# Kernel tuning notes

Measured on AMD Instinct MI355X. Metric: run time of the kernel, lower is better.

Reference implementation:

```python
import jax, jax.numpy as jnp
import numpy as np

B, S = 32, 128
E_NUM, SKILL, D_K, D_E, D_A = 4000, 256, 128, 128, 128
AT_NUM, IT_NUM = 1000, 1000
GAMMA = 0.03


def _lin(key, out_d, in_d):
    # xavier-normal style init
    w = jax.random.normal(key, (out_d, in_d), jnp.float32) * (2.0 / (in_d + out_d)) ** 0.5
    b = jnp.zeros((out_d,), jnp.float32)
    return w, b


def setup_inputs() -> dict:
    key = jax.random.key(0)
    ks = jax.random.split(key, 16)
    exercise_id = jax.random.randint(ks[0], (B, S), 0, E_NUM, jnp.int32)
    ans_time = jax.random.randint(ks[1], (B, S), 0, AT_NUM, jnp.int32)
    interval_time = jax.random.randint(ks[2], (B, S), 0, IT_NUM, jnp.int32)
    answer_value = jax.random.randint(ks[3], (B, S), 0, 2, jnp.int32)
    # enhanced q-matrix: binary with zeros replaced by gamma
    qmask = jax.random.bernoulli(ks[4], 0.1, (E_NUM, SKILL))
    q_matrix = jnp.where(qmask, 1.0, GAMMA).astype(jnp.float32)
    ex_table = jax.random.normal(ks[5], (E_NUM, D_E), jnp.float32)
    at_table = jax.random.normal(ks[6], (AT_NUM, D_K), jnp.float32)
    it_table = jax.random.normal(ks[7], (IT_NUM, D_K), jnp.float32)
    W1, b1 = _lin(ks[8], D_K, D_E + D_K + D_A)   # learning_embed_layer
    Wl, bl = _lin(ks[9], D_K, 4 * D_K)           # learning_layer
    Wg, bg = _lin(ks[10], D_K, 4 * D_K)          # learning_gate
    Wf, bf = _lin(ks[11], D_K, 3 * D_K)          # forgetting_gate
    Wp, bp = _lin(ks[12], D_K, 2 * D_K)          # predicting_layer
    # xavier-uniform initial knowledge state, shared across batch
    lim = (6.0 / (SKILL + D_K)) ** 0.5
    h0 = jax.random.uniform(ks[13], (SKILL, D_K), jnp.float32, -lim, lim)
    return {"exercise_id": exercise_id, "ans_time": ans_time,
            "interval_time": interval_time, "answer_value": answer_value,
            "q_matrix": q_matrix, "ex_table": ex_table, "at_table": at_table,
            "it_table": it_table, "W1": W1, "b1": b1, "Wl": Wl, "bl": bl,
            "Wg": Wg, "bg": bg, "Wf": Wf, "bf": bf, "Wp": Wp, "bp": bp, "h0": h0}


def _forward(exercise_id, ans_time, interval_time, answer_value, q_matrix,
             ex_table, at_table, it_table, W1, b1, Wl, bl, Wg, bg, Wf, bf,
             Wp, bp, h0):
    b, s = exercise_id.shape
    ex = ex_table[exercise_id]                       # (B,S,d_e)
    at = at_table[ans_time]                          # (B,S,d_k)
    it = it_table[interval_time]                     # (B,S,d_k)
    ans = jnp.broadcast_to(answer_value.astype(ex.dtype)[..., None], (b, s, D_A))
    le = jnp.concatenate([ex, at, ans], -1) @ W1.T + b1   # learning embedding (B,S,d_k)
    kv = q_matrix[exercise_id]                       # knowledge vectors (B,S,skill)

    h_pre = jnp.broadcast_to(h0, (b,) + h0.shape)    # (B,skill,d_k)
    h_tilde_pre = jnp.einsum('bs,bsd->bd', kv[:, 0], h_pre)
    learning_pre = jnp.zeros((b, D_K), ex.dtype)

    def step(carry, xs):
        h_pre, h_tilde_pre, learning_pre = carry
        lv, itv, kv_t, kv_next, ex_next = xs
        x4 = jnp.concatenate([learning_pre, itv, lv, h_tilde_pre], -1)
        lg = jnp.tanh(x4 @ Wl.T + bl)
        gate = jax.nn.sigmoid(x4 @ Wg.T + bg)
        LG = gate * (lg + 1.0) * 0.5                 # (B,d_k)
        LG_tilde = kv_t[:, :, None] * LG[:, None, :] # outer product addressing (B,skill,d_k)
        x3 = jnp.concatenate([h_pre,
                              jnp.broadcast_to(LG[:, None, :], h_pre.shape),
                              jnp.broadcast_to(itv[:, None, :], h_pre.shape)], -1)
        f = jax.nn.sigmoid(x3 @ Wf.T + bf)           # forget gate per skill
        h = LG_tilde + f * h_pre                     # updated knowledge state
        h_tilde = jnp.einsum('bs,bsd->bd', kv_next, h)
        pred = jax.nn.sigmoid(jnp.concatenate([ex_next, h_tilde], -1) @ Wp.T + bp)
        return (h, h_tilde, lv), pred

    sw = lambda a: jnp.swapaxes(a, 0, 1)
    xs = (sw(le[:, :-1]), sw(it[:, 1:]), sw(kv[:, :-1]), sw(kv[:, 1:]), sw(ex[:, 1:]))
    _, preds = jax.lax.scan(step, (h_pre, h_tilde_pre, learning_pre), xs)
    return jnp.swapaxes(preds, 0, 1)                 # (B, S-1, d_k)


def reference(exercise_id, ans_time, interval_time, answer_value, q_matrix,
              ex_table, at_table, it_table, W1, b1, Wl, bl, Wg, bg, Wf, bf,
              Wp, bp, h0):
    return _forward(exercise_id, ans_time, interval_time, answer_value, q_matrix,
                    ex_table, at_table, it_table, W1, b1, Wl, bl, Wg, bg, Wf, bf,
                    Wp, bp, h0)
```

## Files before the change

### kernel.cpp

```cpp
#include <hip/hip_runtime.h>

typedef unsigned int u32;
typedef unsigned short u16;
typedef u16 u16x8 __attribute__((ext_vector_type(8)));
typedef u16 u16x4 __attribute__((ext_vector_type(4)));
typedef __bf16 bf16x8 __attribute__((ext_vector_type(8)));
typedef __bf16 bf16x4v __attribute__((ext_vector_type(4)));
typedef float f32x4 __attribute__((ext_vector_type(4)));
typedef float f32x2 __attribute__((ext_vector_type(2)));

#define B_SZ 32
#define S_SZ 128
#define T_SZ 127
#define DK 128
#define SKILL 256
#define SQTR 64
#define RL 136
#define PP 68
#define NPAIR 8

__device__ __forceinline__ u16x4 cvt4(f32x4 v) {
    return __builtin_bit_cast(u16x4, __builtin_convertvector(v, bf16x4v));
}
__device__ __forceinline__ u16x8 cvt8(f32x4 a, f32x4 b) {
    u16x4 x = cvt4(a), y = cvt4(b);
    u16x8 r;
    r[0]=x[0]; r[1]=x[1]; r[2]=x[2]; r[3]=x[3];
    r[4]=y[0]; r[5]=y[1]; r[6]=y[2]; r[7]=y[3];
    return r;
}
__device__ __forceinline__ u16 bfu(float x) {
    return __builtin_bit_cast(u16, (__bf16)x);
}
__device__ __forceinline__ float sigm(float x) {
    float e = __builtin_amdgcn_exp2f(-1.44269504f * x);
    return __builtin_amdgcn_rcpf(1.f + e);
}
__device__ __forceinline__ float tanh_f(float x) {
    float e = __builtin_amdgcn_exp2f(-2.88539008f * x);
    return 2.f * __builtin_amdgcn_rcpf(1.f + e) - 1.f;
}
__device__ __forceinline__ f32x4 mfma16(u16x8 a, u16x8 bb, f32x4 c) {
    return __builtin_amdgcn_mfma_f32_16x16x32_bf16(
        __builtin_bit_cast(bf16x8, a), __builtin_bit_cast(bf16x8, bb), c, 0, 0, 0);
}

__global__ __launch_bounds__(256) void k_le(
    const int* __restrict__ eid, const int* __restrict__ atime,
    const int* __restrict__ ansv, const float* __restrict__ ex_t,
    const float* __restrict__ at_t, const float* __restrict__ W1,
    const float* __restrict__ b1, float* __restrict__ le_ws)
{
    __shared__ float xS[NPAIR * 256];
    __shared__ int   eS[NPAIR], aS[NPAIR];
    __shared__ float avS[NPAIR];
    const int tid = threadIdx.x;
    const int p0 = blockIdx.x * NPAIR;
    if (tid < NPAIR) {
        int p = p0 + tid;
        int b = p / T_SZ, t = p - b * T_SZ;
        eS[tid] = eid[b * S_SZ + t];
        aS[tid] = atime[b * S_SZ + t];
        avS[tid] = (float)ansv[b * S_SZ + t];
    }
    __syncthreads();
    #pragma unroll
    for (int it = 0; it < 2; ++it) {
        int f = it * 256 + tid;
        int pr = f >> 6, c = f & 63;
        const float* src = (c < 32) ? ex_t + eS[pr] * DK + 4 * c
                                    : at_t + aS[pr] * DK + 4 * (c - 32);
        *(f32x4*)(xS + pr * 256 + 4 * c) = *(const f32x4*)src;
    }
    __syncthreads();
    const int o = tid & 127, g = tid >> 7;
    const float* wr = W1 + o * 384;
    const float bias = b1[o];
    float acc[4];
    #pragma unroll
    for (int i = 0; i < 4; ++i) acc[i] = bias;
    #pragma unroll 2
    for (int k4 = 0; k4 < 64; ++k4) {
        f32x4 w = *(const f32x4*)(wr + 4 * k4);
        #pragma unroll
        for (int i = 0; i < 4; ++i) {
            f32x4 x = *(const f32x4*)(xS + (g * 4 + i) * 256 + 4 * k4);
            acc[i] += w[0] * x[0] + w[1] * x[1] + w[2] * x[2] + w[3] * x[3];
        }
    }
    float wsum = 0.f;
    #pragma unroll 4
    for (int k4 = 64; k4 < 96; ++k4) {
        f32x4 w = *(const f32x4*)(wr + 4 * k4);
        wsum += w[0] + w[1] + w[2] + w[3];
    }
    #pragma unroll
    for (int i = 0; i < 4; ++i) {
        int p = p0 + g * 4 + i;
        le_ws[p * DK + o] = acc[i] + avS[g * 4 + i] * wsum;
    }
}

__global__ __launch_bounds__(256) void k_pre(
    const int* __restrict__ itime, const float* __restrict__ it_t,
    const float* __restrict__ Wl, const float* __restrict__ blv,
    const float* __restrict__ Wg, const float* __restrict__ bgv,
    const float* __restrict__ Wf, const float* __restrict__ bfv,
    const float* __restrict__ le_ws,
    float* __restrict__ PRE_l, float* __restrict__ PRE_g, float* __restrict__ PRE_f)
{
    __shared__ float xS[NPAIR * 384];
    __shared__ int ivS[NPAIR], t0S[NPAIR];
    const int tid = threadIdx.x;
    const int p0 = blockIdx.x * NPAIR;
    if (tid < NPAIR) {
        int p = p0 + tid;
        int b = p / T_SZ, t = p - b * T_SZ;
        ivS[tid] = itime[b * S_SZ + t + 1];
        t0S[tid] = (t == 0);
    }
    __syncthreads();
    #pragma unroll
    for (int it = 0; it < 3; ++it) {
        int f = it * 256 + tid;
        int pr = f / 96, c = f - pr * 96;
        int p = p0 + pr;
        f32x4 v;
        if (c < 32) {
            v = t0S[pr] ? (f32x4){0.f, 0.f, 0.f, 0.f}
                        : *(const f32x4*)(le_ws + (p - 1) * DK + 4 * c);
        } else if (c < 64) {
            v = *(const f32x4*)(it_t + ivS[pr] * DK + 4 * (c - 32));
        } else {
            v = *(const f32x4*)(le_ws + p * DK + 4 * (c - 64));
        }
        *(f32x4*)(xS + pr * 384 + 4 * c) = v;
    }
    __syncthreads();
    const int o = tid & 127, g = tid >> 7;
    const float* wl = Wl + o * 512;
    const float* wg = Wg + o * 512;
    const float bl0 = blv[o], bg0 = bgv[o];
    float al[4], ag[4];
    #pragma unroll
    for (int i = 0; i < 4; ++i) { al[i] = bl0; ag[i] = bg0; }
    #pragma unroll 2
    for (int k4 = 0; k4 < 96; ++k4) {
        f32x4 w  = *(const f32x4*)(wl + 4 * k4);
        f32x4 w2 = *(const f32x4*)(wg + 4 * k4);
        #pragma unroll
        for (int i = 0; i < 4; ++i) {
            f32x4 x = *(const f32x4*)(xS + (g * 4 + i) * 384 + 4 * k4);
            al[i] += w[0] * x[0] + w[1] * x[1] + w[2] * x[2] + w[3] * x[3];
            ag[i] += w2[0] * x[0] + w2[1] * x[1] + w2[2] * x[2] + w2[3] * x[3];
        }
    }
    const float bf0 = bfv[o];
    float af[4];
    #pragma unroll
    for (int i = 0; i < 4; ++i) af[i] = bf0;
    const float* wf = Wf + o * 384 + 256;
    #pragma unroll 2
    for (int k4 = 0; k4 < 32; ++k4) {
        f32x4 w = *(const f32x4*)(wf + 4 * k4);
        #pragma unroll
        for (int i = 0; i < 4; ++i) {
            f32x4 x = *(const f32x4*)(xS + (g * 4 + i) * 384 + 128 + 4 * k4);
            af[i] += w[0] * x[0] + w[1] * x[1] + w[2] * x[2] + w[3] * x[3];
        }
    }
    #pragma unroll
    for (int i = 0; i < 4; ++i) {
        size_t idx = (size_t)(p0 + g * 4 + i) * DK + o;
        PRE_l[idx] = al[i];
        PRE_g[idx] = ag[i];
        PRE_f[idx] = af[i];
    }
}

__global__ __launch_bounds__(512, 1) void k_main(
    const int* __restrict__ eid, const float* __restrict__ qmat,
    const float* __restrict__ Wl, const float* __restrict__ Wg,
    const float* __restrict__ Wf, const float* __restrict__ h0,
    const float* __restrict__ PRE_l, const float* __restrict__ PRE_g,
    const float* __restrict__ PRE_f, float* __restrict__ ht_ws,
    float* __restrict__ xbuf, int* __restrict__ flags)
{
    extern __shared__ char smem[];
    u16*   hS   = (u16*)smem;
    float* part = (float*)(smem + 17408);
    u16*   htbf = (u16*)(smem + 52224);
    u16*   LGb  = (u16*)(smem + 52736);
    float* LGf  = (float*)(smem + 53248);
    float* cS   = (float*)(smem + 53760);

    const int b    = blockIdx.x;
    const int qid  = blockIdx.y;
    const int tid  = threadIdx.x;
    const int w    = tid >> 6;
    const int lane = tid & 63;
    const int quad = lane >> 4;
    const int l4   = lane & 15;
    const int ih   = w & 1;
    const int jh   = w >> 1;

    float* xb  = xbuf  + b * 1024;
    int*   flg = flags + b * 32;

    const int pq = (lane < 3) ? ((lane < qid) ? lane : lane + 1) : qid;

    u16x8 afr[4][4];
    #pragma unroll
    for (int mt = 0; mt < 4; ++mt)
        #pragma unroll
        for (int kt = 0; kt < 4; ++kt) {
            const float* p = Wf + (64 * ih + 16 * mt + l4) * 384 + 32 * kt + quad * 8;
            afr[mt][kt] = cvt8(*(const f32x4*)p, *(const f32x4*)(p + 4));
        }
    u16x8 azf[2][4];
    #pragma unroll
    for (int mt = 0; mt < 2; ++mt)
        #pragma unroll
        for (int kt = 0; kt < 4; ++kt) {
            int d = 16 * w + 8 * mt + (l4 >> 1);
            const float* base = (l4 & 1) ? Wg : Wl;
            const float* p = base + d * 512 + 384 + 32 * kt + quad * 8;
            azf[mt][kt] = cvt8(*(const f32x4*)p, *(const f32x4*)(p + 4));
        }
    u16x8 acf[4];
    #pragma unroll
    for (int kt = 0; kt < 4; ++kt) {
        const float* p = Wf + (16 * w + l4) * 384 + 128 + 32 * kt + quad * 8;
        acf[kt] = cvt8(*(const f32x4*)p, *(const f32x4*)(p + 4));
    }

    const int sl = 16 * jh + l4;
    f32x4 hreg[4];
    #pragma unroll
    for (int mt = 0; mt < 4; ++mt) {
        int d0 = 64 * ih + 16 * mt + quad * 4;
        f32x4 hv = *(const f32x4*)(h0 + (SQTR * qid + sl) * DK + d0);
        hreg[mt] = hv;
        *(u16x4*)(hS + sl * RL + d0) = cvt4(hv);
    }

    float kvt = qmat[eid[b * S_SZ] * SKILL + SQTR * qid + sl];

    f32x4 accF[4];

    {
        float htp[16];
        #pragma unroll
        for (int mt = 0; mt < 4; ++mt)
            #pragma unroll
            for (int r = 0; r < 4; ++r)
                htp[mt * 4 + r] = kvt * hreg[mt][r];
        #pragma unroll
        for (int mt = 0; mt < 4; ++mt)
            #pragma unroll
            for (int r = 0; r < 4; ++r)
                part[(64 * ih + 16 * mt + quad * 4 + r) * PP + jh * 16 + l4] = htp[mt * 4 + r];
        __syncthreads();
        int d = tid >> 2, kq = tid & 3;
        const float* pp = part + d * PP + kq * 16;
        float v = 0.f;
        #pragma unroll
        for (int i4 = 0; i4 < 4; ++i4) {
            f32x4 x = *(const f32x4*)(pp + 4 * i4);
            v += x[0] + x[1] + x[2] + x[3];
        }
        v += __shfl_xor(v, 1, 64);
        v += __shfl_xor(v, 2, 64);
        if (kq == 0)
            __hip_atomic_store(xb + (qid * 2 + 1) * 128 + d, v,
                               __ATOMIC_RELAXED, __HIP_MEMORY_SCOPE_AGENT);
        asm volatile("s_waitcnt vmcnt(0)" ::: "memory");
        if (lane == 0)
            __hip_atomic_store(flg + qid * 8 + w, 1,
                               __ATOMIC_RELAXED, __HIP_MEMORY_SCOPE_AGENT);
        #pragma unroll
        for (int mt = 0; mt < 4; ++mt)
            accF[mt] = (f32x4){0.f, 0.f, 0.f, 0.f};
        {
            const u16* bp = hS + sl * RL + quad * 8;
            u16x8 bfr[4];
            #pragma unroll
            for (int kt = 0; kt < 4; ++kt) bfr[kt] = *(const u16x8*)(bp + kt * 32);
            #pragma unroll
            for (int mt = 0; mt < 4; ++mt)
                #pragma unroll
                for (int kt = 0; kt < 4; ++kt)
                    accF[mt] = mfma16(afr[mt][kt], bfr[kt], accF[mt]);
        }
        {
            int spins = 0;
            while (true) {
                int fv = __hip_atomic_load(flg + pq * 8 + w,
                                           __ATOMIC_RELAXED, __HIP_MEMORY_SCOPE_AGENT);
                if (__all(fv >= 1)) break;
                __builtin_amdgcn_s_sleep(1);
                if (++spins > (1 << 20)) break;
            }
        }
        asm volatile("" ::: "memory");
        if (kq == 0) {
            float q0 = (qid == 0) ? v : __hip_atomic_load(xb + (0 * 2 + 1) * 128 + d, __ATOMIC_RELAXED, __HIP_MEMORY_SCOPE_AGENT);
            float q1 = (qid == 1) ? v : __hip_atomic_load(xb + (1 * 2 + 1) * 128 + d, __ATOMIC_RELAXED, __HIP_MEMORY_SCOPE_AGENT);
            float q2 = (qid == 2) ? v : __hip_atomic_load(xb + (2 * 2 + 1) * 128 + d, __ATOMIC_RELAXED, __HIP_MEMORY_SCOPE_AGENT);
            float q3 = (qid == 3) ? v : __hip_atomic_load(xb + (3 * 2 + 1) * 128 + d, __ATOMIC_RELAXED, __HIP_MEMORY_SCOPE_AGENT);
            float vt = ((q0 + q1) + q2) + q3;
            float hf = (float)(__bf16)vt;
            htbf[d] = bfu(vt);
            htbf[128 + d] = bfu(vt - hf);
        }
        __syncthreads();
    }

    for (int t = 0; t < T_SZ; ++t) {
        const size_t tb = (size_t)(b * T_SZ + t) * DK;
        float kvn = qmat[eid[b * S_SZ + t + 1] * SKILL + SQTR * qid + sl];
        f32x2 pl[2], pg[2];
        #pragma unroll
        for (int mt = 0; mt < 2; ++mt) {
            int d0 = 16 * w + 8 * mt + 2 * quad;
            pl[mt] = *(const f32x2*)(PRE_l + tb + d0);
            pg[mt] = *(const f32x2*)(PRE_g + tb + d0);
        }
        f32x4 pf = *(const f32x4*)(PRE_f + tb + 16 * w + quad * 4);

        f32x4 accZ[2];
        accZ[0] = (f32x4){0.f, 0.f, 0.f, 0.f};
        accZ[1] = (f32x4){0.f, 0.f, 0.f, 0.f};
        #pragma unroll
        for (int kt = 0; kt < 4; ++kt) {
            u16x8 bh = *(const u16x8*)(htbf + 32 * kt + quad * 8);
            u16x8 bl = *(const u16x8*)(htbf + 128 + 32 * kt + quad * 8);
            #pragma unroll
            for (int mt = 0; mt < 2; ++mt) {
                accZ[mt] = mfma16(azf[mt][kt], bh, accZ[mt]);
                accZ[mt] = mfma16(azf[mt][kt], bl, accZ[mt]);
            }
        }
        #pragma unroll
        for (int mt = 0; mt < 2; ++mt) {
            u32 hpack = 0, lpack = 0;
            f32x2 fpack;
            #pragma unroll
            for (int rp = 0; rp < 2; ++rp) {
                float zl = accZ[mt][2 * rp] + pl[mt][rp];
                float zg = accZ[mt][2 * rp + 1] + pg[mt][rp];
                float LGv = sigm(zg) * (tanh_f(zl) + 1.f) * 0.5f;
                float hif = (float)(__bf16)LGv;
                hpack |= ((u32)bfu(LGv)) << (16 * rp);
                lpack |= ((u32)bfu(LGv - hif)) << (16 * rp);
                fpack[rp] = LGv;
            }
            if (l4 == 0) {
                int d0 = 16 * w + 8 * mt + 2 * quad;
                *(u32*)(LGb + d0) = hpack;
                *(u32*)(LGb + 128 + d0) = lpack;
                *(f32x2*)(LGf + d0) = fpack;
            }
        }
        __syncthreads();

        {
            f32x4 accC = (f32x4){0.f, 0.f, 0.f, 0.f};
            #pragma unroll
            for (int kt = 0; kt < 4; ++kt) {
                u16x8 bh = *(const u16x8*)(LGb + 32 * kt + quad * 8);
                u16x8 bl = *(const u16x8*)(LGb + 128 + 32 * kt + quad * 8);
                accC = mfma16(acf[kt], bh, accC);
                accC = mfma16(acf[kt], bl, accC);
            }
            accC += pf;
            if (l4 == 0) *(f32x4*)(cS + 16 * w + quad * 4) = accC;
        }
        __syncthreads();

        float htp[16];
        #pragma unroll
        for (int mt = 0; mt < 4; ++mt) {
            int d0 = 64 * ih + 16 * mt + quad * 4;
            f32x4 lg = *(const f32x4*)(LGf + d0);
            f32x4 cc = *(const f32x4*)(cS + d0);
            f32x4 hv;
            #pragma unroll
            for (int r = 0; r < 4; ++r) {
                float f = sigm(accF[mt][r] + cc[r]);
                float hn = kvt * lg[r] + f * hreg[mt][r];
                hreg[mt][r] = hn;
                htp[mt * 4 + r] = kvn * hn;
                hv[r] = hn;
            }
            *(u16x4*)(hS + sl * RL + d0) = cvt4(hv);
        }
        #pragma unroll
        for (int mt = 0; mt < 4; ++mt)
            #pragma unroll
            for (int r = 0; r < 4; ++r)
                part[(64 * ih + 16 * mt + quad * 4 + r) * PP + jh * 16 + l4] = htp[mt * 4 + r];
        kvt = kvn;
        __syncthreads();

        {
            int d = tid >> 2, kq = tid & 3;
            const float* pp = part + d * PP + kq * 16;
            float v = 0.f;
            #pragma unroll
            for (int i4 = 0; i4 < 4; ++i4) {
                f32x4 x = *(const f32x4*)(pp + 4 * i4);
                v += x[0] + x[1] + x[2] + x[3];
            }
            v += __shfl_xor(v, 1, 64);
            v += __shfl_xor(v, 2, 64);
            int slot = t & 1;
            if (kq == 0)
                __hip_atomic_store(xb + (qid * 2 + slot) * 128 + d, v,
                                   __ATOMIC_RELAXED, __HIP_MEMORY_SCOPE_AGENT);
            asm volatile("s_waitcnt vmcnt(0)" ::: "memory");
            if (lane == 0)
                __hip_atomic_store(flg + qid * 8 + w, t + 2,
                                   __ATOMIC_RELAXED, __HIP_MEMORY_SCOPE_AGENT);
            #pragma unroll
            for (int mt = 0; mt < 4; ++mt)
                accF[mt] = (f32x4){0.f, 0.f, 0.f, 0.f};
            {
                const u16* bp = hS + sl * RL + quad * 8;
                u16x8 bfr[4];
                #pragma unroll
                for (int kt = 0; kt < 4; ++kt) bfr[kt] = *(const u16x8*)(bp + kt * 32);
                #pragma unroll
                for (int mt = 0; mt < 4; ++mt)
                    #pragma unroll
                    for (int kt = 0; kt < 4; ++kt)
                        accF[mt] = mfma16(afr[mt][kt], bfr[kt], accF[mt]);
            }
            {
                int spins = 0;
                while (true) {
                    int fv = __hip_atomic_load(flg + pq * 8 + w,
                                               __ATOMIC_RELAXED, __HIP_MEMORY_SCOPE_AGENT);
                    if (__all(fv >= t + 2)) break;
                    __builtin_amdgcn_s_sleep(1);
                    if (++spins > (1 << 20)) break;
                }
            }
            asm volatile("" ::: "memory");
            if (kq == 0) {
                float q0 = (qid == 0) ? v : __hip_atomic_load(xb + (0 * 2 + slot) * 128 + d, __ATOMIC_RELAXED, __HIP_MEMORY_SCOPE_AGENT);
                float q1 = (qid == 1) ? v : __hip_atomic_load(xb + (1 * 2 + slot) * 128 + d, __ATOMIC_RELAXED, __HIP_MEMORY_SCOPE_AGENT);
                float q2 = (qid == 2) ? v : __hip_atomic_load(xb + (2 * 2 + slot) * 128 + d, __ATOMIC_RELAXED, __HIP_MEMORY_SCOPE_AGENT);
                float q3 = (qid == 3) ? v : __hip_atomic_load(xb + (3 * 2 + slot) * 128 + d, __ATOMIC_RELAXED, __HIP_MEMORY_SCOPE_AGENT);
                float vt = ((q0 + q1) + q2) + q3;
                float hf = (float)(__bf16)vt;
                htbf[d] = bfu(vt);
                htbf[128 + d] = bfu(vt - hf);
                if (qid == 0) ht_ws[tb + d] = vt;
            }
        }
        __syncthreads();
    }
}

__global__ __launch_bounds__(256) void k_pred(
    const int* __restrict__ eid, const float* __restrict__ ex_t,
    const float* __restrict__ Wp, const float* __restrict__ bpv,
    const float* __restrict__ ht_ws, float* __restrict__ out)
{
    __shared__ float xS[NPAIR * 256];
    __shared__ int eS[NPAIR];
    const int tid = threadIdx.x;
    const int p0 = blockIdx.x * NPAIR;
    if (tid < NPAIR) {
        int p = p0 + tid;
        int b = p / T_SZ, t = p - b * T_SZ;
        eS[tid] = eid[b * S_SZ + t + 1];
    }
    __syncthreads();
    #pragma unroll
    for (int it = 0; it < 2; ++it) {
        int f = it * 256 + tid;
        int pr = f >> 6, c = f & 63;
        const float* src = (c < 32) ? ex_t + eS[pr] * DK + 4 * c
                                    : ht_ws + (size_t)(p0 + pr) * DK + 4 * (c - 32);
        *(f32x4*)(xS + pr * 256 + 4 * c) = *(const f32x4*)src;
    }
    __syncthreads();
    const int o = tid & 127, g = tid >> 7;
    const float* wr = Wp + o * 256;
    const float bias = bpv[o];
    float acc[4];
    #pragma unroll
    for (int i = 0; i < 4; ++i) acc[i] = bias;
    #pragma unroll 2
    for (int k4 = 0; k4 < 64; ++k4) {
        f32x4 w = *(const f32x4*)(wr + 4 * k4);
        #pragma unroll
        for (int i = 0; i < 4; ++i) {
            f32x4 x = *(const f32x4*)(xS + (g * 4 + i) * 256 + 4 * k4);
            acc[i] += w[0] * x[0] + w[1] * x[1] + w[2] * x[2] + w[3] * x[3];
        }
    }
    #pragma unroll
    for (int i = 0; i < 4; ++i)
        out[(size_t)(p0 + g * 4 + i) * DK + o] = sigm(acc[i]);
}

extern "C" void kernel_launch(void* const* d_in, const int* in_sizes, int n_in,
                              void* d_out, int out_size, void* d_ws, size_t ws_size,
                              hipStream_t stream) {
    const int* eid     = (const int*)d_in[0];
    const int* atime   = (const int*)d_in[1];
    const int* itime   = (const int*)d_in[2];
    const int* ansv    = (const int*)d_in[3];
    const float* qmat  = (const float*)d_in[4];
    const float* ex_t  = (const float*)d_in[5];
    const float* at_t  = (const float*)d_in[6];
    const float* it_t  = (const float*)d_in[7];
    const float* W1    = (const float*)d_in[8];
    const float* b1    = (const float*)d_in[9];
    const float* Wl    = (const float*)d_in[10];
    const float* blv   = (const float*)d_in[11];
    const float* Wg    = (const float*)d_in[12];
    const float* bgv   = (const float*)d_in[13];
    const float* Wf    = (const float*)d_in[14];
    const float* bfv   = (const float*)d_in[15];
    const float* Wp    = (const float*)d_in[16];
    const float* bpv   = (const float*)d_in[17];
    const float* h0    = (const float*)d_in[18];
    float* out = (float*)d_out;

    const size_t SZ = (size_t)B_SZ * T_SZ * DK;
    float* wsf   = (float*)d_ws;
    float* le_ws = wsf;
    float* PRE_l = wsf + SZ;
    float* PRE_g = wsf + 2 * SZ;
    float* PRE_f = wsf + 3 * SZ;
    float* ht_ws = wsf + 4 * SZ;
    float* xbuf  = le_ws;
    int*   flags = (int*)(le_ws + 32768);

    hipFuncSetAttribute((const void*)k_main,
                        hipFuncAttributeMaxDynamicSharedMemorySize, 86016);

    dim3 gaux(508);
    k_le  <<<gaux, 256, 0, stream>>>(eid, atime, ansv, ex_t, at_t, W1, b1, le_ws);
    k_pre <<<gaux, 256, 0, stream>>>(itime, it_t, Wl, blv, Wg, bgv, Wf, bfv,
                                     le_ws, PRE_l, PRE_g, PRE_f);
    hipMemsetAsync(flags, 0, 32 * 32 * sizeof(int), stream);
    k_main<<<dim3(B_SZ, 4), 512, 86016, stream>>>(eid, qmat, Wl, Wg, Wf, h0,
                                                  PRE_l, PRE_g, PRE_f, ht_ws,
                                                  xbuf, flags);
    k_pred<<<gaux, 256, 0, stream>>>(eid, ex_t, Wp, bpv, ht_ws, out);
}
```

Before: 693.1 us.

## Pack sequence tags with values for cross-block exchange; drop LDS staging

The cross-block partial-sum exchange in the recurrent kernel now writes 64-bit packets that carry a sequence number beside the float value. Consumers spin directly on the data words, which removes the separate flag stores, the vmcnt drain and the wave-wide flag polling on every timestep. The spin also busy-polls for a short while before it starts sleeping. Separately, the auxiliary linear kernels stop staging inputs in shared memory and read the gathered rows straight from global memory with uniform per-wave indices. This relies on 64-bit relaxed atomics being single-copy atomic, and it clears a larger exchange buffer with the memset.

```diff
diff --git a/kernel.cpp b/kernel.cpp
--- a/kernel.cpp
+++ b/kernel.cpp
@@ -2,6 +2,7 @@
 
 typedef unsigned int u32;
 typedef unsigned short u16;
+typedef unsigned long long u64;
 typedef u16 u16x8 __attribute__((ext_vector_type(8)));
 typedef u16 u16x4 __attribute__((ext_vector_type(4)));
 typedef __bf16 bf16x8 __attribute__((ext_vector_type(8)));
@@ -18,6 +19,7 @@
 #define RL 136
 #define PP 68
 #define NPAIR 8
+#define SPIN_CAP (1 << 18)
 
 __device__ __forceinline__ u16x4 cvt4(f32x4 v) {
     return __builtin_bit_cast(u16x4, __builtin_convertvector(v, bf16x4v));
@@ -44,6 +46,9 @@
     return __builtin_amdgcn_mfma_f32_16x16x32_bf16(
         __builtin_bit_cast(bf16x8, a), __builtin_bit_cast(bf16x8, bb), c, 0, 0, 0);
 }
+__device__ __forceinline__ float pval(u64 p) {
+    return __builtin_bit_cast(float, (u32)p);
+}
 
 __global__ __launch_bounds__(256) void k_le(
     const int* __restrict__ eid, const int* __restrict__ atime,
@@ -51,40 +56,38 @@
     const float* __restrict__ at_t, const float* __restrict__ W1,
     const float* __restrict__ b1, float* __restrict__ le_ws)
 {
-    __shared__ float xS[NPAIR * 256];
-    __shared__ int   eS[NPAIR], aS[NPAIR];
-    __shared__ float avS[NPAIR];
     const int tid = threadIdx.x;
-    const int p0 = blockIdx.x * NPAIR;
-    if (tid < NPAIR) {
-        int p = p0 + tid;
-        int b = p / T_SZ, t = p - b * T_SZ;
-        eS[tid] = eid[b * S_SZ + t];
-        aS[tid] = atime[b * S_SZ + t];
-        avS[tid] = (float)ansv[b * S_SZ + t];
-    }
-    __syncthreads();
-    #pragma unroll
-    for (int it = 0; it < 2; ++it) {
-        int f = it * 256 + tid;
-        int pr = f >> 6, c = f & 63;
-        const float* src = (c < 32) ? ex_t + eS[pr] * DK + 4 * c
-                                    : at_t + aS[pr] * DK + 4 * (c - 32);
-        *(f32x4*)(xS + pr * 256 + 4 * c) = *(const f32x4*)src;
-    }
-    __syncthreads();
-    const int o = tid & 127, g = tid >> 7;
+    const int o = tid & 127;
+    const int gi = __builtin_amdgcn_readfirstlane(tid >> 7);
+    const int p0 = blockIdx.x * NPAIR + gi * 4;
+    int eP[4], aP[4];
+    float avP[4];
+    #pragma unroll
+    for (int i = 0; i < 4; ++i) {
+        int p = p0 + i, b = p / T_SZ, t = p - b * T_SZ;
+        int idx = b * S_SZ + t;
+        eP[i] = eid[idx];
+        aP[i] = atime[idx];
+        avP[i] = (float)ansv[idx];
+    }
     const float* wr = W1 + o * 384;
     const float bias = b1[o];
-    float acc[4];
-    #pragma unroll
-    for (int i = 0; i < 4; ++i) acc[i] = bias;
-    #pragma unroll 2
-    for (int k4 = 0; k4 < 64; ++k4) {
+    float acc[4] = {bias, bias, bias, bias};
+    #pragma unroll 4
+    for (int k4 = 0; k4 < 32; ++k4) {
         f32x4 w = *(const f32x4*)(wr + 4 * k4);
         #pragma unroll
         for (int i = 0; i < 4; ++i) {
-            f32x4 x = *(const f32x4*)(xS + (g * 4 + i) * 256 + 4 * k4);
+            f32x4 x = *(const f32x4*)(ex_t + eP[i] * DK + 4 * k4);
+            acc[i] += w[0] * x[0] + w[1] * x[1] + w[2] * x[2] + w[3] * x[3];
+        }
+    }
+    #pragma unroll 4
+    for (int k4 = 32; k4 < 64; ++k4) {
+        f32x4 w = *(const f32x4*)(wr + 4 * k4);
+        #pragma unroll
+        for (int i = 0; i < 4; ++i) {
+            f32x4 x = *(const f32x4*)(at_t + aP[i] * DK + 4 * k4 - 128);
             acc[i] += w[0] * x[0] + w[1] * x[1] + w[2] * x[2] + w[3] * x[3];
         }
     }
@@ -95,10 +98,8 @@
         wsum += w[0] + w[1] + w[2] + w[3];
     }
     #pragma unroll
-    for (int i = 0; i < 4; ++i) {
-        int p = p0 + g * 4 + i;
-        le_ws[p * DK + o] = acc[i] + avS[g * 4 + i] * wsum;
-    }
+    for (int i = 0; i < 4; ++i)
+        le_ws[(p0 + i) * DK + o] = acc[i] + avP[i] * wsum;
 }
 
 __global__ __launch_bounds__(256) void k_pre(
@@ -109,69 +110,82 @@
     const float* __restrict__ le_ws,
     float* __restrict__ PRE_l, float* __restrict__ PRE_g, float* __restrict__ PRE_f)
 {
-    __shared__ float xS[NPAIR * 384];
-    __shared__ int ivS[NPAIR], t0S[NPAIR];
     const int tid = threadIdx.x;
-    const int p0 = blockIdx.x * NPAIR;
-    if (tid < NPAIR) {
-        int p = p0 + tid;
-        int b = p / T_SZ, t = p - b * T_SZ;
-        ivS[tid] = itime[b * S_SZ + t + 1];
-        t0S[tid] = (t == 0);
-    }
-    __syncthreads();
-    #pragma unroll
-    for (int it = 0; it < 3; ++it) {
-        int f = it * 256 + tid;
-        int pr = f / 96, c = f - pr * 96;
-        int p = p0 + pr;
-        f32x4 v;
-        if (c < 32) {
-            v = t0S[pr] ? (f32x4){0.f, 0.f, 0.f, 0.f}
-                        : *(const f32x4*)(le_ws + (p - 1) * DK + 4 * c);
-        } else if (c < 64) {
-            v = *(const f32x4*)(it_t + ivS[pr] * DK + 4 * (c - 32));
-        } else {
-            v = *(const f32x4*)(le_ws + p * DK + 4 * (c - 64));
-        }
-        *(f32x4*)(xS + pr * 384 + 4 * c) = v;
-    }
-    __syncthreads();
-    const int o = tid & 127, g = tid >> 7;
+    const int o = tid & 127;
+    const int gi = __builtin_amdgcn_readfirstlane(tid >> 7);
+    const int p0 = blockIdx.x * NPAIR + gi * 4;
+    int ivP[4], lpOff[4];
+    float mP[4];
+    #pragma unroll
+    for (int i = 0; i < 4; ++i) {
+        int p = p0 + i, b = p / T_SZ, t = p - b * T_SZ;
+        ivP[i] = itime[b * S_SZ + t + 1];
+        mP[i] = (t == 0) ? 0.f : 1.f;
+        lpOff[i] = ((t == 0) ? p : p - 1) * DK;
+    }
     const float* wl = Wl + o * 512;
     const float* wg = Wg + o * 512;
     const float bl0 = blv[o], bg0 = bgv[o];
-    float al[4], ag[4];
-    #pragma unroll
-    for (int i = 0; i < 4; ++i) { al[i] = bl0; ag[i] = bg0; }
-    #pragma unroll 2
-    for (int k4 = 0; k4 < 96; ++k4) {
+    float al[4] = {bl0, bl0, bl0, bl0};
+    float ag[4] = {bg0, bg0, bg0, bg0};
+    #pragma unroll 4
+    for (int k4 = 0; k4 < 32; ++k4) {
         f32x4 w  = *(const f32x4*)(wl + 4 * k4);
         f32x4 w2 = *(const f32x4*)(wg + 4 * k4);
         #pragma unroll
         for (int i = 0; i < 4; ++i) {
-            f32x4 x = *(const f32x4*)(xS + (g * 4 + i) * 384 + 4 * k4);
-            al[i] += w[0] * x[0] + w[1] * x[1] + w[2] * x[2] + w[3] * x[3];
-            ag[i] += w2[0] * x[0] + w2[1] * x[1] + w2[2] * x[2] + w2[3] * x[3];
+            f32x4 x = *(const f32x4*)(le_ws + lpOff[i] + 4 * k4);
+            #pragma unroll
+            for (int j = 0; j < 4; ++j) {
+                float xv = x[j] * mP[i];
+                al[i] += w[j] * xv;
+                ag[i] += w2[j] * xv;
+            }
+        }
+    }
+    #pragma unroll 4
+    for (int k4 = 0; k4 < 32; ++k4) {
+        f32x4 w  = *(const f32x4*)(wl + 128 + 4 * k4);
+        f32x4 w2 = *(const f32x4*)(wg + 128 + 4 * k4);
+        #pragma unroll
+        for (int i = 0; i < 4; ++i) {
+            f32x4 x = *(const f32x4*)(it_t + ivP[i] * DK + 4 * k4);
+            #pragma unroll
+            for (int j = 0; j < 4; ++j) {
+                al[i] += w[j] * x[j];
+                ag[i] += w2[j] * x[j];
+            }
+        }
+    }
+    #pragma unroll 4
+    for (int k4 = 0; k4 < 32; ++k4) {
+        f32x4 w  = *(const f32x4*)(wl + 256 + 4 * k4);
+        f32x4 w2 = *(const f32x4*)(wg + 256 + 4 * k4);
+        #pragma unroll
+        for (int i = 0; i < 4; ++i) {
+            f32x4 x = *(const f32x4*)(le_ws + (p0 + i) * DK + 4 * k4);
+            #pragma unroll
+            for (int j = 0; j < 4; ++j) {
+                al[i] += w[j] * x[j];
+                ag[i] += w2[j] * x[j];
+            }
         }
     }
     const float bf0 = bfv[o];
-    float af[4];
-    #pragma unroll
-    for (int i = 0; i < 4; ++i) af[i] = bf0;
+    float af[4] = {bf0, bf0, bf0, bf0};
     const float* wf = Wf + o * 384 + 256;
-    #pragma unroll 2
+    #pragma unroll 4
     for (int k4 = 0; k4 < 32; ++k4) {
         f32x4 w = *(const f32x4*)(wf + 4 * k4);
         #pragma unroll
         for (int i = 0; i < 4; ++i) {
-            f32x4 x = *(const f32x4*)(xS + (g * 4 + i) * 384 + 128 + 4 * k4);
+            f32x4 x = *(const f32x4*)(it_t + ivP[i] * DK + 4 * k4);
             af[i] += w[0] * x[0] + w[1] * x[1] + w[2] * x[2] + w[3] * x[3];
         }
     }
     #pragma unroll
     for (int i = 0; i < 4; ++i) {
-        size_t idx = (size_t)(p0 + g * 4 + i) * DK + o;
+        size_t idx = (size_t)(p0 + i) * DK + o;
         PRE_l[idx] = al[i];
         PRE_g[idx] = ag[i];
         PRE_f[idx] = af[i];
@@ -184,7 +198,7 @@
     const float* __restrict__ Wf, const float* __restrict__ h0,
     const float* __restrict__ PRE_l, const float* __restrict__ PRE_g,
     const float* __restrict__ PRE_f, float* __restrict__ ht_ws,
-    float* __restrict__ xbuf, int* __restrict__ flags)
+    u64* __restrict__ xbuf)
 {
     extern __shared__ char smem[];
     u16*   hS   = (u16*)smem;
@@ -204,10 +218,8 @@
     const int ih   = w & 1;
     const int jh   = w >> 1;
 
-    float* xb  = xbuf  + b * 1024;
-    int*   flg = flags + b * 32;
-
-    const int pq = (lane < 3) ? ((lane < qid) ? lane : lane + 1) : qid;
+    u64* xq = xbuf + (size_t)b * 1024;
+    const int qa = (qid + 1) & 3, qb2 = (qid + 2) & 3, qc = (qid + 3) & 3;
 
     u16x8 afr[4][4];
     #pragma unroll
@@ -271,13 +283,12 @@
         }
         v += __shfl_xor(v, 1, 64);
         v += __shfl_xor(v, 2, 64);
-        if (kq == 0)
-            __hip_atomic_store(xb + (qid * 2 + 1) * 128 + d, v,
+        if (kq == 0) {
+            u64 pkt = ((u64)1u << 32) | (u64)__builtin_bit_cast(u32, v);
+            __hip_atomic_store(xq + qid * 256 + 128 + d, pkt,
                                __ATOMIC_RELAXED, __HIP_MEMORY_SCOPE_AGENT);
-        asm volatile("s_waitcnt vmcnt(0)" ::: "memory");
-        if (lane == 0)
-            __hip_atomic_store(flg + qid * 8 + w, 1,
-                               __ATOMIC_RELAXED, __HIP_MEMORY_SCOPE_AGENT);
+        }
+        asm volatile("" ::: "memory");
         #pragma unroll
         for (int mt = 0; mt < 4; ++mt)
             accF[mt] = (f32x4){0.f, 0.f, 0.f, 0.f};
@@ -292,23 +303,22 @@
                 for (int kt = 0; kt < 4; ++kt)
                     accF[mt] = mfma16(afr[mt][kt], bfr[kt], accF[mt]);
         }
-        {
+        if (kq == 0) {
+            u64 pa, pb, pc;
             int spins = 0;
-            while (true) {
-                int fv = __hip_atomic_load(flg + pq * 8 + w,
-                                           __ATOMIC_RELAXED, __HIP_MEMORY_SCOPE_AGENT);
-                if (__all(fv >= 1)) break;
-                __builtin_amdgcn_s_sleep(1);
-                if (++spins > (1 << 20)) break;
-            }
-        }
-        asm volatile("" ::: "memory");
-        if (kq == 0) {
-            float q0 = (qid == 0) ? v : __hip_atomic_load(xb + (0 * 2 + 1) * 128 + d, __ATOMIC_RELAXED, __HIP_MEMORY_SCOPE_AGENT);
-            float q1 = (qid == 1) ? v : __hip_atomic_load(xb + (1 * 2 + 1) * 128 + d, __ATOMIC_RELAXED, __HIP_MEMORY_SCOPE_AGENT);
-            float q2 = (qid == 2) ? v : __hip_atomic_load(xb + (2 * 2 + 1) * 128 + d, __ATOMIC_RELAXED, __HIP_MEMORY_SCOPE_AGENT);
-            float q3 = (qid == 3) ? v : __hip_atomic_load(xb + (3 * 2 + 1) * 128 + d, __ATOMIC_RELAXED, __HIP_MEMORY_SCOPE_AGENT);
-            float vt = ((q0 + q1) + q2) + q3;
+            do {
+                pa = __hip_atomic_load(xq + qa * 256 + 128 + d, __ATOMIC_RELAXED, __HIP_MEMORY_SCOPE_AGENT);
+                pb = __hip_atomic_load(xq + qb2 * 256 + 128 + d, __ATOMIC_RELAXED, __HIP_MEMORY_SCOPE_AGENT);
+                pc = __hip_atomic_load(xq + qc * 256 + 128 + d, __ATOMIC_RELAXED, __HIP_MEMORY_SCOPE_AGENT);
+                if ((u32)(pa >> 32) >= 1u && (u32)(pb >> 32) >= 1u && (u32)(pc >> 32) >= 1u) break;
+                if (spins > 64) __builtin_amdgcn_s_sleep(1);
+            } while (++spins < SPIN_CAP);
+            float va = pval(pa), vb = pval(pb), vc = pval(pc);
+            float v0 = (qid == 0) ? v : (qid == 3) ? va : (qid == 2) ? vb : vc;
+            float v1 = (qid == 1) ? v : (qid == 0) ? va : (qid == 3) ? vb : vc;
+            float v2 = (qid == 2) ? v : (qid == 1) ? va : (qid == 0) ? vb : vc;
+            float v3 = (qid == 3) ? v : (qid == 2) ? va : (qid == 1) ? vb : vc;
+            float vt = ((v0 + v1) + v2) + v3;
             float hf = (float)(__bf16)vt;
             htbf[d] = bfu(vt);
             htbf[128 + d] = bfu(vt - hf);
@@ -414,14 +424,14 @@
             }
             v += __shfl_xor(v, 1, 64);
             v += __shfl_xor(v, 2, 64);
-            int slot = t & 1;
-            if (kq == 0)
-                __hip_atomic_store(xb + (qid * 2 + slot) * 128 + d, v,
+            const int slot = t & 1;
+            const u32 seq = (u32)(t + 2);
+            if (kq == 0) {
+                u64 pkt = ((u64)seq << 32) | (u64)__builtin_bit_cast(u32, v);
+                __hip_atomic_store(xq + qid * 256 + slot * 128 + d, pkt,
                                    __ATOMIC_RELAXED, __HIP_MEMORY_SCOPE_AGENT);
-            asm volatile("s_waitcnt vmcnt(0)" ::: "memory");
-            if (lane == 0)
-                __hip_atomic_store(flg + qid * 8 + w, t + 2,
-                                   __ATOMIC_RELAXED, __HIP_MEMORY_SCOPE_AGENT);
+            }
+            asm volatile("" ::: "memory");
             #pragma unroll
             for (int mt = 0; mt < 4; ++mt)
                 accF[mt] = (f32x4){0.f, 0.f, 0.f, 0.f};
@@ -436,23 +446,22 @@
                     for (int kt = 0; kt < 4; ++kt)
                         accF[mt] = mfma16(afr[mt][kt], bfr[kt], accF[mt]);
             }
-            {
+            if (kq == 0) {
+                u64 pa, pb, pc;
                 int spins = 0;
-                while (true) {
-                    int fv = __hip_atomic_load(flg + pq * 8 + w,
-                                               __ATOMIC_RELAXED, __HIP_MEMORY_SCOPE_AGENT);
-                    if (__all(fv >= t + 2)) break;
-                    __builtin_amdgcn_s_sleep(1);
-                    if (++spins > (1 << 20)) break;
-                }
-            }
-            asm volatile("" ::: "memory");
-            if (kq == 0) {
-                float q0 = (qid == 0) ? v : __hip_atomic_load(xb + (0 * 2 + slot) * 128 + d, __ATOMIC_RELAXED, __HIP_MEMORY_SCOPE_AGENT);
-                float q1 = (qid == 1) ? v : __hip_atomic_load(xb + (1 * 2 + slot) * 128 + d, __ATOMIC_RELAXED, __HIP_MEMORY_SCOPE_AGENT);
-                float q2 = (qid == 2) ? v : __hip_atomic_load(xb + (2 * 2 + slot) * 128 + d, __ATOMIC_RELAXED, __HIP_MEMORY_SCOPE_AGENT);
-                float q3 = (qid == 3) ? v : __hip_atomic_load(xb + (3 * 2 + slot) * 128 + d, __ATOMIC_RELAXED, __HIP_MEMORY_SCOPE_AGENT);
-                float vt = ((q0 + q1) + q2) + q3;
+                do {
+                    pa = __hip_atomic_load(xq + qa * 256 + slot * 128 + d, __ATOMIC_RELAXED, __HIP_MEMORY_SCOPE_AGENT);
+                    pb = __hip_atomic_load(xq + qb2 * 256 + slot * 128 + d, __ATOMIC_RELAXED, __HIP_MEMORY_SCOPE_AGENT);
+                    pc = __hip_atomic_load(xq + qc * 256 + slot * 128 + d, __ATOMIC_RELAXED, __HIP_MEMORY_SCOPE_AGENT);
+                    if ((u32)(pa >> 32) >= seq && (u32)(pb >> 32) >= seq && (u32)(pc >> 32) >= seq) break;
+                    if (spins > 64) __builtin_amdgcn_s_sleep(1);
+                } while (++spins < SPIN_CAP);
+                float va = pval(pa), vb = pval(pb), vc = pval(pc);
+                float v0 = (qid == 0) ? v : (qid == 3) ? va : (qid == 2) ? vb : vc;
+                float v1 = (qid == 1) ? v : (qid == 0) ? va : (qid == 3) ? vb : vc;
+                float v2 = (qid == 2) ? v : (qid == 1) ? va : (qid == 0) ? vb : vc;
+                float v3 = (qid == 3) ? v : (qid == 2) ? va : (qid == 1) ? vb : vc;
+                float vt = ((v0 + v1) + v2) + v3;
                 float hf = (float)(__bf16)vt;
                 htbf[d] = bfu(vt);
                 htbf[128 + d] = bfu(vt - hf);
@@ -468,43 +477,40 @@
     const float* __restrict__ Wp, const float* __restrict__ bpv,
     const float* __restrict__ ht_ws, float* __restrict__ out)
 {
-    __shared__ float xS[NPAIR * 256];
-    __shared__ int eS[NPAIR];
     const int tid = threadIdx.x;
-    const int p0 = blockIdx.x * NPAIR;
-    if (tid < NPAIR) {
-        int p = p0 + tid;
-        int b = p / T_SZ, t = p - b * T_SZ;
-        eS[tid] = eid[b * S_SZ + t + 1];
-    }
-    __syncthreads();
-    #pragma unroll
-    for (int it = 0; it < 2; ++it) {
-        int f = it * 256 + tid;
-        int pr = f >> 6, c = f & 63;
-        const float* src = (c < 32) ? ex_t + eS[pr] * DK + 4 * c
-                                    : ht_ws + (size_t)(p0 + pr) * DK + 4 * (c - 32);
-        *(f32x4*)(xS + pr * 256 + 4 * c) = *(const f32x4*)src;
-    }
-    __syncthreads();
-    const int o = tid & 127, g = tid >> 7;
+    const int o = tid & 127;
+    const int gi = __builtin_amdgcn_readfirstlane(tid >> 7);
+    const int p0 = blockIdx.x * NPAIR + gi * 4;
+    int eP[4];
+    #pragma unroll
+    for (int i = 0; i < 4; ++i) {
+        int p = p0 + i, b = p / T_SZ, t = p - b * T_SZ;
+        eP[i] = eid[b * S_SZ + t + 1];
+    }
     const float* wr = Wp + o * 256;
     const float bias = bpv[o];
-    float acc[4];
-    #pragma unroll
-    for (int i = 0; i < 4; ++i) acc[i] = bias;
-    #pragma unroll 2
-    for (int k4 = 0; k4 < 64; ++k4) {
+    float acc[4] = {bias, bias, bias, bias};
+    #pragma unroll 4
+    for (int k4 = 0; k4 < 32; ++k4) {
         f32x4 w = *(const f32x4*)(wr + 4 * k4);
         #pragma unroll
         for (int i = 0; i < 4; ++i) {
-            f32x4 x = *(const f32x4*)(xS + (g * 4 + i) * 256 + 4 * k4);
+            f32x4 x = *(const f32x4*)(ex_t + eP[i] * DK + 4 * k4);
             acc[i] += w[0] * x[0] + w[1] * x[1] + w[2] * x[2] + w[3] * x[3];
         }
     }
+    #pragma unroll 4
+    for (int k4 = 32; k4 < 64; ++k4) {
+        f32x4 w = *(const f32x4*)(wr + 4 * k4);
+        #pragma unroll
+        for (int i = 0; i < 4; ++i) {
+            f32x4 x = *(const f32x4*)(ht_ws + (size_t)(p0 + i) * DK + 4 * k4 - 128);
+            acc[i] += w[0] * x[0] + w[1] * x[1] + w[2] * x[2] + w[3] * x[3];
+        }
+    }
     #pragma unroll
     for (int i = 0; i < 4; ++i)
-        out[(size_t)(p0 + g * 4 + i) * DK + o] = sigm(acc[i]);
+        out[(size_t)(p0 + i) * DK + o] = sigm(acc[i]);
 }
 
 extern "C" void kernel_launch(void* const* d_in, const int* in_sizes, int n_in,
@@ -538,8 +544,7 @@
     float* PRE_g = wsf + 2 * SZ;
     float* PRE_f = wsf + 3 * SZ;
     float* ht_ws = wsf + 4 * SZ;
-    float* xbuf  = le_ws;
-    int*   flags = (int*)(le_ws + 32768);
+    u64* xbuf = (u64*)le_ws;
 
     hipFuncSetAttribute((const void*)k_main,
                         hipFuncAttributeMaxDynamicSharedMemorySize, 86016);
@@ -548,9 +553,9 @@
     k_le  <<<gaux, 256, 0, stream>>>(eid, atime, ansv, ex_t, at_t, W1, b1, le_ws);
     k_pre <<<gaux, 256, 0, stream>>>(itime, it_t, Wl, blv, Wg, bgv, Wf, bfv,
                                      le_ws, PRE_l, PRE_g, PRE_f);
-    hipMemsetAsync(flags, 0, 32 * 32 * sizeof(int), stream);
+    hipMemsetAsync(xbuf, 0, (size_t)B_SZ * 1024 * sizeof(u64), stream);
     k_main<<<dim3(B_SZ, 4), 512, 86016, stream>>>(eid, qmat, Wl, Wg, Wf, h0,
                                                   PRE_l, PRE_g, PRE_f, ht_ws,
-                                                  xbuf, flags);
+                                                  xbuf);
     k_pred<<<gaux, 256, 0, stream>>>(eid, ex_t, Wp, bpv, ht_ws, out);
 }
```

Result: faster. 593.6 us (median of 2 runs) (-14.3%).
